# Performance work log

Measured on AMD Instinct MI355X. Metric: run time of the kernel, lower is better.

Reference implementation:

```python
import jax, jax.numpy as jnp
import numpy as np

B, T, D = 4, 2048, 1024
H = 16
HD = D // H

def setup_inputs() -> dict:
    key = jax.random.key(0)
    k1, k2, k3, k4, k5 = jax.random.split(key, 5)
    x = jax.random.normal(k1, (B, T, D), dtype=jnp.float32)
    scale = 1.0 / np.sqrt(D)
    W_qkv = jax.random.normal(k2, (D, 3 * D), dtype=jnp.float32) * scale
    b_qkv = jnp.zeros((3 * D,), dtype=jnp.float32)
    W_proj = jax.random.normal(k3, (D, D), dtype=jnp.float32) * scale
    b_proj = jnp.zeros((D,), dtype=jnp.float32)
    return {"x": x, "W_qkv": W_qkv, "b_qkv": b_qkv, "W_proj": W_proj, "b_proj": b_proj}

def reference(x, W_qkv, b_qkv, W_proj, b_proj):
    Bx, Tx, C = x.shape
    qkv = x @ W_qkv + b_qkv                      # [B,T,3C]
    q, k, v = jnp.split(qkv, 3, axis=-1)
    # [B,T,H,hd] -> [B,H,T,hd]
    q = q.reshape(Bx, Tx, H, HD).transpose(0, 2, 1, 3)
    k = k.reshape(Bx, Tx, H, HD).transpose(0, 2, 1, 3)
    v = v.reshape(Bx, Tx, H, HD).transpose(0, 2, 1, 3)
    att = jnp.einsum('bhqd,bhkd->bhqk', q, k) / jnp.sqrt(jnp.float32(HD))
    causal = jnp.tril(jnp.ones((Tx, Tx), dtype=bool))
    att = jnp.where(causal[None, None], att, -jnp.inf)
    att = jax.nn.softmax(att, axis=-1)
    y = jnp.einsum('bhqk,bhkd->bhqd', att, v)    # [B,H,T,hd]
    y = y.transpose(0, 2, 1, 3).reshape(Bx, Tx, C)
    return y @ W_proj + b_proj
```

## Files before the change

### kernel.cpp

```cpp
#include <hip/hip_runtime.h>
#include <hip/hip_bf16.h>

#define B_  4
#define T_  2048
#define D_  1024
#define H_  16
#define HD_ 64

typedef short s16x8 __attribute__((ext_vector_type(8)));
typedef short s16x4 __attribute__((ext_vector_type(4)));
typedef float f32x4 __attribute__((ext_vector_type(4)));
typedef unsigned int u32x2 __attribute__((ext_vector_type(2)));

#define MFMA32(a, b, c) __builtin_amdgcn_mfma_f32_16x16x32_bf16(a, b, c, 0, 0, 0)
#define MFMA16(a, b, c) __builtin_amdgcn_mfma_f32_16x16x16bf16_1k(a, b, c, 0, 0, 0)

__device__ __forceinline__ unsigned short f2bf(float f) {
  unsigned u = __builtin_bit_cast(unsigned, f);
  u += 0x7fffu + ((u >> 16) & 1u);
  return (unsigned short)(u >> 16);
}

__device__ __forceinline__ float bf2f(unsigned short h) {
  return __builtin_bit_cast(float, (unsigned)h << 16);
}

#define GLOAD_LDS16(src, dst)                                            \
  __builtin_amdgcn_global_load_lds(                                      \
      (__attribute__((address_space(1))) void*)(void*)(src),             \
      (__attribute__((address_space(3))) void*)(dst), 16, 0, 0)

__global__ __launch_bounds__(256) void convert_x_kernel(
    const float* __restrict__ in, unsigned short* __restrict__ out, int n8) {
  int i = blockIdx.x * 256 + threadIdx.x;
  if (i >= n8) return;
  const float4* p = ((const float4*)in) + (size_t)i * 2;
  float4 a = p[0], b = p[1];
  s16x8 o;
  o[0] = (short)f2bf(a.x); o[1] = (short)f2bf(a.y);
  o[2] = (short)f2bf(a.z); o[3] = (short)f2bf(a.w);
  o[4] = (short)f2bf(b.x); o[5] = (short)f2bf(b.y);
  o[6] = (short)f2bf(b.z); o[7] = (short)f2bf(b.w);
  *(((s16x8*)out) + i) = o;
}

__global__ __launch_bounds__(256) void transpose_w_kernel(
    const float* __restrict__ W, unsigned short* __restrict__ Wt, int K, int N) {
  __shared__ float tile[32][33];
  int n0 = blockIdx.x * 32, k0 = blockIdx.y * 32;
  int tx = threadIdx.x & 31, ty = threadIdx.x >> 5;
#pragma unroll
  for (int j = 0; j < 4; ++j) {
    int k = ty + j * 8;
    tile[k][tx] = W[(size_t)(k0 + k) * N + n0 + tx];
  }
  __syncthreads();
#pragma unroll
  for (int j = 0; j < 4; ++j) {
    int n = ty + j * 8;
    Wt[(size_t)(n0 + n) * K + k0 + tx] = f2bf(tile[tx][n]);
  }
}

template <int OUTF32>
__global__ __launch_bounds__(256) void gemm_kernel(
    const unsigned short* __restrict__ A, const unsigned short* __restrict__ Bt,
    const float* __restrict__ bias, void* __restrict__ Cout, int M, int N, int K) {
  __shared__ char lds[32768];
  char* Al = lds;
  char* Bl = lds + 16384;
  const int n0 = blockIdx.x * 128, m0 = blockIdx.y * 128;
  const int w = threadIdx.x >> 6, lane = threadIdx.x & 63;
  const int l15 = lane & 15, g = lane >> 4;
  const int wr = w >> 1, wc = w & 1;
  const int srow = (lane >> 3);
  const int u = lane & 7;
  f32x4 acc[4][4] = {};

  for (int kt = 0; kt < K; kt += 64) {
    __syncthreads();
#pragma unroll
    for (int i = 0; i < 4; ++i) {
      int c = w * 4 + i;
      int row = c * 8 + srow;
      const unsigned short* srcA = A + (size_t)(m0 + row) * K + kt + u * 8;
      GLOAD_LDS16(srcA, Al + c * 1024);
      const unsigned short* srcB = Bt + (size_t)(n0 + row) * K + kt + u * 8;
      GLOAD_LDS16(srcB, Bl + c * 1024);
    }
    __syncthreads();
#pragma unroll
    for (int kk = 0; kk < 2; ++kk) {
      s16x8 af[4], bfr[4];
#pragma unroll
      for (int mi = 0; mi < 4; ++mi) {
        int row = wr * 64 + mi * 16 + l15;
        af[mi] = *(const s16x8*)(Al + row * 128 + kk * 64 + g * 16);
      }
#pragma unroll
      for (int ni = 0; ni < 4; ++ni) {
        int row = wc * 64 + ni * 16 + l15;
        bfr[ni] = *(const s16x8*)(Bl + row * 128 + kk * 64 + g * 16);
      }
#pragma unroll
      for (int mi = 0; mi < 4; ++mi)
#pragma unroll
        for (int ni = 0; ni < 4; ++ni)
          acc[mi][ni] = MFMA32(af[mi], bfr[ni], acc[mi][ni]);
    }
  }
#pragma unroll
  for (int ni = 0; ni < 4; ++ni) {
    int col = n0 + wc * 64 + ni * 16 + l15;
    float bv = bias[col];
#pragma unroll
    for (int mi = 0; mi < 4; ++mi) {
      int row = m0 + wr * 64 + mi * 16 + g * 4;
#pragma unroll
      for (int r = 0; r < 4; ++r) {
        float v = acc[mi][ni][r] + bv;
        if (OUTF32)
          ((float*)Cout)[(size_t)(row + r) * N + col] = v;
        else
          ((unsigned short*)Cout)[(size_t)(row + r) * N + col] = f2bf(v);
      }
    }
  }
}

__global__ __launch_bounds__(256, 4) void attn_kernel(
    const unsigned short* __restrict__ qkv, unsigned short* __restrict__ yatt) {
  __shared__ char lds[8192 + 9344];
  const int bx = blockIdx.x;
  const int bh = blockIdx.y;
  const int b = bh >> 4, h = bh & 15;
  const int w = threadIdx.x >> 6;
  const int lane = threadIdx.x & 63;
  const int l15 = lane & 15, g = lane >> 4;

  const size_t rowstride = 3 * D_;
  const unsigned short* Qb = qkv + (size_t)b * T_ * rowstride + h * HD_;
  const unsigned short* Kb = Qb + D_;
  const unsigned short* Vb = Qb + 2 * D_;

  char* Klds = lds;
  unsigned short* Vt = (unsigned short*)(lds + 8192);

  const int krow0 = (w * 2 + 0) * 8 + (lane >> 3);
  const int krow1 = (w * 2 + 1) * 8 + (lane >> 3);
  const int u = lane & 7;
  const int vkey = w * 16 + (lane >> 2);
  const int vdb = lane & 3;
  const float SC = 0.18033688011112042f;

  s16x8 kreg0, kreg1, vreg0, vreg1;
  auto load_kv = [&](int kt) {
    const unsigned short* kb = Kb + (size_t)(kt * 64) * rowstride;
    kreg0 = *(const s16x8*)(kb + (size_t)krow0 * rowstride + u * 8);
    kreg1 = *(const s16x8*)(kb + (size_t)krow1 * rowstride + u * 8);
    const unsigned short* vs = Vb + (size_t)(kt * 64 + vkey) * rowstride + vdb * 16;
    vreg0 = *(const s16x8*)(vs);
    vreg1 = *(const s16x8*)(vs + 8);
  };

  load_kv(0);
#pragma unroll 1
  for (int ti = 0; ti < 2; ++ti) {
    const int qt = ti ? bx : 31 - bx;
    s16x8 qf0, qf1;
    {
      const unsigned short* qr = Qb + (size_t)(qt * 64 + w * 16 + l15) * rowstride;
      s16x8 a0 = *(const s16x8*)(qr + g * 8);
      s16x8 a1 = *(const s16x8*)(qr + 32 + g * 8);
#pragma unroll
      for (int j = 0; j < 8; ++j) {
        qf0[j] = (short)f2bf(bf2f((unsigned short)a0[j]) * SC);
        qf1[j] = (short)f2bf(bf2f((unsigned short)a1[j]) * SC);
      }
    }
    float m = -1e30f, rs = 0.f;
    f32x4 acc[4] = {};

#pragma unroll 1
    for (int kt = 0; kt <= qt; ++kt) {
      __syncthreads();
      *(s16x8*)(Klds + krow0 * 128 + ((u ^ (krow0 & 7)) << 4)) = kreg0;
      *(s16x8*)(Klds + krow1 * 128 + ((u ^ (krow1 & 7)) << 4)) = kreg1;
#pragma unroll
      for (int j = 0; j < 8; ++j) {
        Vt[vdb * 1168 + j * 72 + vkey] = (unsigned short)vreg0[j];
        Vt[vdb * 1168 + (8 + j) * 72 + vkey] = (unsigned short)vreg1[j];
      }
      __syncthreads();
      if (kt < qt) load_kv(kt + 1);
      else if (ti == 0) load_kv(0);

      float tv[16];
#pragma unroll
      for (int kk = 0; kk < 4; ++kk) {
        int key = kk * 16 + l15;
        const s16x8 kf0 = *(const s16x8*)(Klds + key * 128 + ((g ^ (key & 7)) << 4));
        const s16x8 kf1 = *(const s16x8*)(Klds + key * 128 + (((4 + g) ^ (key & 7)) << 4));
        f32x4 s = {};
        s = MFMA32(kf0, qf0, s);
        s = MFMA32(kf1, qf1, s);
#pragma unroll
        for (int r = 0; r < 4; ++r) tv[kk * 4 + r] = s[r];
      }
      if (kt == qt) {
        int q = qt * 64 + w * 16 + l15;
#pragma unroll
        for (int kk = 0; kk < 4; ++kk)
#pragma unroll
          for (int r = 0; r < 4; ++r)
            if (kt * 64 + kk * 16 + g * 4 + r > q) tv[kk * 4 + r] = -1e30f;
      }
      float tm = tv[0];
#pragma unroll
      for (int i = 1; i < 16; ++i) tm = fmaxf(tm, tv[i]);
      tm = fmaxf(tm, __shfl_xor(tm, 16));
      tm = fmaxf(tm, __shfl_xor(tm, 32));
      if (!__all(tm - m <= 8.0f)) {
        float mn = fmaxf(m, tm);
        float corr = exp2f(m - mn);
        m = mn;
        rs *= corr;
#pragma unroll
        for (int i = 0; i < 4; ++i) {
          acc[i][0] *= corr; acc[i][1] *= corr; acc[i][2] *= corr; acc[i][3] *= corr;
        }
      }
      s16x4 pb[4];
      float ps = 0.f;
#pragma unroll
      for (int kk = 0; kk < 4; ++kk) {
        float p0 = exp2f(tv[kk * 4 + 0] - m), p1 = exp2f(tv[kk * 4 + 1] - m);
        float p2 = exp2f(tv[kk * 4 + 2] - m), p3 = exp2f(tv[kk * 4 + 3] - m);
        ps += (p0 + p1) + (p2 + p3);
        u32x2 pk;
        pk[0] = __builtin_amdgcn_perm(__builtin_bit_cast(unsigned, p1),
                                      __builtin_bit_cast(unsigned, p0), 0x07060302u);
        pk[1] = __builtin_amdgcn_perm(__builtin_bit_cast(unsigned, p3),
                                      __builtin_bit_cast(unsigned, p2), 0x07060302u);
        pb[kk] = __builtin_bit_cast(s16x4, pk);
      }
      rs += ps;
#pragma unroll
      for (int kk = 0; kk < 4; ++kk) {
#pragma unroll
        for (int db = 0; db < 4; ++db) {
          s16x4 vf = *(const s16x4*)(Vt + db * 1168 + l15 * 72 + kk * 16 + g * 4);
          acc[db] = MFMA16(vf, pb[kk], acc[db]);
        }
      }
    }

    float rtot = rs + __shfl_xor(rs, 16);
    rtot += __shfl_xor(rtot, 32);
    float inv = 1.0f / rtot;
    __syncthreads();
    unsigned short* ylds = (unsigned short*)lds;
#pragma unroll
    for (int db = 0; db < 4; ++db)
#pragma unroll
      for (int r = 0; r < 4; ++r)
        ylds[(db * 16 + g * 4 + r) * 66 + w * 16 + l15] = f2bf(acc[db][r] * inv);
    __syncthreads();
    int qq = threadIdx.x >> 2;
    int dc = (threadIdx.x & 3) * 16;
    s16x8 o1, o2;
#pragma unroll
    for (int j = 0; j < 8; ++j) {
      o1[j] = (short)ylds[(dc + j) * 66 + qq];
      o2[j] = (short)ylds[(dc + 8 + j) * 66 + qq];
    }
    unsigned short* dst = yatt + (size_t)(b * T_ + qt * 64 + qq) * D_ + h * HD_ + dc;
    *(s16x8*)(dst) = o1;
    *(s16x8*)(dst + 8) = o2;
  }
}

extern "C" void kernel_launch(void* const* d_in, const int* in_sizes, int n_in,
                              void* d_out, int out_size, void* d_ws, size_t ws_size,
                              hipStream_t stream) {
  const float* x     = (const float*)d_in[0];
  const float* Wqkv  = (const float*)d_in[1];
  const float* bqkv  = (const float*)d_in[2];
  const float* Wproj = (const float*)d_in[3];
  const float* bproj = (const float*)d_in[4];
  float* out = (float*)d_out;

  unsigned short* xb   = (unsigned short*)d_ws;
  unsigned short* Wqb  = xb + (size_t)8192 * 1024;
  unsigned short* Wpb  = Wqb + (size_t)3072 * 1024;
  unsigned short* qkvb = Wpb + (size_t)1024 * 1024;
  unsigned short* yb   = xb;

  convert_x_kernel<<<dim3(4096), dim3(256), 0, stream>>>(x, xb, 8192 * 1024 / 8);
  transpose_w_kernel<<<dim3(96, 32), dim3(256), 0, stream>>>(Wqkv, Wqb, 1024, 3072);
  transpose_w_kernel<<<dim3(32, 32), dim3(256), 0, stream>>>(Wproj, Wpb, 1024, 1024);
  gemm_kernel<0><<<dim3(24, 64), dim3(256), 0, stream>>>(xb, Wqb, bqkv, qkvb, 8192, 3072, 1024);
  attn_kernel<<<dim3(16, 64), dim3(256), 0, stream>>>(qkvb, yb);
  gemm_kernel<1><<<dim3(8, 64), dim3(256), 0, stream>>>(yb, Wpb, bproj, out, 8192, 1024, 1024);
}
```

Baseline: 210.0 us.

## Widen attention query tile to 128 rows with 8 waves sharing each K/V tile

New measurement: 393.8 us. 87.5% more time.

```diff
diff --git a/kernel.cpp b/kernel.cpp
--- a/kernel.cpp
+++ b/kernel.cpp
@@ -128,14 +128,16 @@
   }
 }
 
-__global__ __launch_bounds__(256, 4) void attn_kernel(
+#define VT_STR 66
+__global__ __launch_bounds__(512, 4) void attn_kernel(
     const unsigned short* __restrict__ qkv, unsigned short* __restrict__ yatt) {
-  __shared__ char lds[8192 + 9344];
+  __shared__ char lds[16640];
   const int bx = blockIdx.x;
   const int bh = blockIdx.y;
   const int b = bh >> 4, h = bh & 15;
-  const int w = threadIdx.x >> 6;
-  const int lane = threadIdx.x & 63;
+  const int tid = threadIdx.x;
+  const int w = tid >> 6;
+  const int lane = tid & 63;
   const int l15 = lane & 15, g = lane >> 4;
 
   const size_t rowstride = 3 * D_;
@@ -146,30 +148,25 @@
   char* Klds = lds;
   unsigned short* Vt = (unsigned short*)(lds + 8192);
 
-  const int krow0 = (w * 2 + 0) * 8 + (lane >> 3);
-  const int krow1 = (w * 2 + 1) * 8 + (lane >> 3);
-  const int u = lane & 7;
-  const int vkey = w * 16 + (lane >> 2);
-  const int vdb = lane & 3;
+  const int srow = tid >> 3;
+  const int oct = tid & 7;
+  const int koff0 = (g ^ (l15 & 7)) << 4;
+  const int koff1 = ((4 + g) ^ (l15 & 7)) << 4;
   const float SC = 0.18033688011112042f;
 
-  s16x8 kreg0, kreg1, vreg0, vreg1;
+  s16x8 kreg, vreg;
   auto load_kv = [&](int kt) {
-    const unsigned short* kb = Kb + (size_t)(kt * 64) * rowstride;
-    kreg0 = *(const s16x8*)(kb + (size_t)krow0 * rowstride + u * 8);
-    kreg1 = *(const s16x8*)(kb + (size_t)krow1 * rowstride + u * 8);
-    const unsigned short* vs = Vb + (size_t)(kt * 64 + vkey) * rowstride + vdb * 16;
-    vreg0 = *(const s16x8*)(vs);
-    vreg1 = *(const s16x8*)(vs + 8);
+    kreg = *(const s16x8*)(Kb + (size_t)(kt * 64 + srow) * rowstride + oct * 8);
+    vreg = *(const s16x8*)(Vb + (size_t)(kt * 64 + srow) * rowstride + oct * 8);
   };
 
   load_kv(0);
 #pragma unroll 1
   for (int ti = 0; ti < 2; ++ti) {
-    const int qt = ti ? bx : 31 - bx;
+    const int qt = ti ? bx : 15 - bx;
     s16x8 qf0, qf1;
     {
-      const unsigned short* qr = Qb + (size_t)(qt * 64 + w * 16 + l15) * rowstride;
+      const unsigned short* qr = Qb + (size_t)(qt * 128 + w * 16 + l15) * rowstride;
       s16x8 a0 = *(const s16x8*)(qr + g * 8);
       s16x8 a1 = *(const s16x8*)(qr + 32 + g * 8);
 #pragma unroll
@@ -180,77 +177,84 @@
     }
     float m = -1e30f, rs = 0.f;
     f32x4 acc[4] = {};
+    const int ktmax = 2 * qt + 1;
 
 #pragma unroll 1
-    for (int kt = 0; kt <= qt; ++kt) {
+    for (int kt = 0; kt <= ktmax; ++kt) {
       __syncthreads();
-      *(s16x8*)(Klds + krow0 * 128 + ((u ^ (krow0 & 7)) << 4)) = kreg0;
-      *(s16x8*)(Klds + krow1 * 128 + ((u ^ (krow1 & 7)) << 4)) = kreg1;
-#pragma unroll
-      for (int j = 0; j < 8; ++j) {
-        Vt[vdb * 1168 + j * 72 + vkey] = (unsigned short)vreg0[j];
-        Vt[vdb * 1168 + (8 + j) * 72 + vkey] = (unsigned short)vreg1[j];
-      }
+      *(s16x8*)(Klds + srow * 128 + ((oct ^ (srow & 7)) << 4)) = kreg;
+#pragma unroll
+      for (int j = 0; j < 8; ++j)
+        Vt[(oct * 8 + j) * VT_STR + srow] = (unsigned short)vreg[j];
       __syncthreads();
-      if (kt < qt) load_kv(kt + 1);
+      if (kt < ktmax) load_kv(kt + 1);
       else if (ti == 0) load_kv(0);
 
-      float tv[16];
-#pragma unroll
-      for (int kk = 0; kk < 4; ++kk) {
-        int key = kk * 16 + l15;
-        const s16x8 kf0 = *(const s16x8*)(Klds + key * 128 + ((g ^ (key & 7)) << 4));
-        const s16x8 kf1 = *(const s16x8*)(Klds + key * 128 + (((4 + g) ^ (key & 7)) << 4));
-        f32x4 s = {};
-        s = MFMA32(kf0, qf0, s);
-        s = MFMA32(kf1, qf1, s);
-#pragma unroll
-        for (int r = 0; r < 4; ++r) tv[kk * 4 + r] = s[r];
-      }
-      if (kt == qt) {
-        int q = qt * 64 + w * 16 + l15;
-#pragma unroll
-        for (int kk = 0; kk < 4; ++kk)
-#pragma unroll
-          for (int r = 0; r < 4; ++r)
-            if (kt * 64 + kk * 16 + g * 4 + r > q) tv[kk * 4 + r] = -1e30f;
-      }
-      float tm = tv[0];
-#pragma unroll
-      for (int i = 1; i < 16; ++i) tm = fmaxf(tm, tv[i]);
-      tm = fmaxf(tm, __shfl_xor(tm, 16));
-      tm = fmaxf(tm, __shfl_xor(tm, 32));
-      if (!__all(tm - m <= 8.0f)) {
-        float mn = fmaxf(m, tm);
-        float corr = exp2f(m - mn);
-        m = mn;
-        rs *= corr;
-#pragma unroll
-        for (int i = 0; i < 4; ++i) {
-          acc[i][0] *= corr; acc[i][1] *= corr; acc[i][2] *= corr; acc[i][3] *= corr;
-        }
-      }
-      s16x4 pb[4];
-      float ps = 0.f;
-#pragma unroll
-      for (int kk = 0; kk < 4; ++kk) {
-        float p0 = exp2f(tv[kk * 4 + 0] - m), p1 = exp2f(tv[kk * 4 + 1] - m);
-        float p2 = exp2f(tv[kk * 4 + 2] - m), p3 = exp2f(tv[kk * 4 + 3] - m);
-        ps += (p0 + p1) + (p2 + p3);
-        u32x2 pk;
-        pk[0] = __builtin_amdgcn_perm(__builtin_bit_cast(unsigned, p1),
-                                      __builtin_bit_cast(unsigned, p0), 0x07060302u);
-        pk[1] = __builtin_amdgcn_perm(__builtin_bit_cast(unsigned, p3),
-                                      __builtin_bit_cast(unsigned, p2), 0x07060302u);
-        pb[kk] = __builtin_bit_cast(s16x4, pk);
-      }
-      rs += ps;
-#pragma unroll
-      for (int kk = 0; kk < 4; ++kk) {
-#pragma unroll
-        for (int db = 0; db < 4; ++db) {
-          s16x4 vf = *(const s16x4*)(Vt + db * 1168 + l15 * 72 + kk * 16 + g * 4);
-          acc[db] = MFMA16(vf, pb[kk], acc[db]);
+      const bool skip = (kt * 64 > qt * 128 + w * 16 + 15);
+      if (!skip) {
+        float tv[16];
+        const char* kbase = Klds + l15 * 128;
+#pragma unroll
+        for (int kk = 0; kk < 4; ++kk) {
+          const s16x8 kf0 = *(const s16x8*)(kbase + kk * 2048 + koff0);
+          const s16x8 kf1 = *(const s16x8*)(kbase + kk * 2048 + koff1);
+          f32x4 s = {};
+          s = MFMA32(kf0, qf0, s);
+          s = MFMA32(kf1, qf1, s);
+#pragma unroll
+          for (int r = 0; r < 4; ++r) tv[kk * 4 + r] = s[r];
+        }
+        if (kt * 64 + 63 > qt * 128 + w * 16) {
+          int q = qt * 128 + w * 16 + l15;
+#pragma unroll
+          for (int kk = 0; kk < 4; ++kk)
+#pragma unroll
+            for (int r = 0; r < 4; ++r)
+              if (kt * 64 + kk * 16 + g * 4 + r > q) tv[kk * 4 + r] = -1e30f;
+        }
+        float x0 = fmaxf(tv[0], tv[1]), x1 = fmaxf(tv[2], tv[3]);
+        float x2 = fmaxf(tv[4], tv[5]), x3 = fmaxf(tv[6], tv[7]);
+        float x4 = fmaxf(tv[8], tv[9]), x5 = fmaxf(tv[10], tv[11]);
+        float x6 = fmaxf(tv[12], tv[13]), x7 = fmaxf(tv[14], tv[15]);
+        float y0 = fmaxf(fmaxf(x0, x1), fmaxf(x2, x3));
+        float y1 = fmaxf(fmaxf(x4, x5), fmaxf(x6, x7));
+        float tm = fmaxf(y0, y1);
+        tm = fmaxf(tm, __shfl_xor(tm, 16));
+        tm = fmaxf(tm, __shfl_xor(tm, 32));
+        if (!__all(tm - m <= 8.0f)) {
+          float mn = fmaxf(m, tm);
+          float corr = exp2f(m - mn);
+          m = mn;
+          rs *= corr;
+#pragma unroll
+          for (int i = 0; i < 4; ++i) {
+            acc[i][0] *= corr; acc[i][1] *= corr;
+            acc[i][2] *= corr; acc[i][3] *= corr;
+          }
+        }
+        s16x4 pb[4];
+        float ps = 0.f;
+#pragma unroll
+        for (int kk = 0; kk < 4; ++kk) {
+          float p0 = exp2f(tv[kk * 4 + 0] - m), p1 = exp2f(tv[kk * 4 + 1] - m);
+          float p2 = exp2f(tv[kk * 4 + 2] - m), p3 = exp2f(tv[kk * 4 + 3] - m);
+          ps += (p0 + p1) + (p2 + p3);
+          u32x2 pk;
+          pk[0] = __builtin_amdgcn_perm(__builtin_bit_cast(unsigned, p1),
+                                        __builtin_bit_cast(unsigned, p0), 0x07060302u);
+          pk[1] = __builtin_amdgcn_perm(__builtin_bit_cast(unsigned, p3),
+                                        __builtin_bit_cast(unsigned, p2), 0x07060302u);
+          pb[kk] = __builtin_bit_cast(s16x4, pk);
+        }
+        rs += ps;
+#pragma unroll
+        for (int kk = 0; kk < 4; ++kk) {
+#pragma unroll
+          for (int db = 0; db < 4; ++db) {
+            s16x4 vf =
+                *(const s16x4*)(Vt + (db * 16 + l15) * VT_STR + kk * 16 + g * 4);
+            acc[db] = MFMA16(vf, pb[kk], acc[db]);
+          }
         }
       }
     }
@@ -264,19 +268,22 @@
     for (int db = 0; db < 4; ++db)
 #pragma unroll
       for (int r = 0; r < 4; ++r)
-        ylds[(db * 16 + g * 4 + r) * 66 + w * 16 + l15] = f2bf(acc[db][r] * inv);
+        ylds[(db * 16 + g * 4 + r) * 130 + w * 16 + l15] = f2bf(acc[db][r] * inv);
     __syncthreads();
-    int qq = threadIdx.x >> 2;
-    int dc = (threadIdx.x & 3) * 16;
-    s16x8 o1, o2;
-#pragma unroll
-    for (int j = 0; j < 8; ++j) {
-      o1[j] = (short)ylds[(dc + j) * 66 + qq];
-      o2[j] = (short)ylds[(dc + 8 + j) * 66 + qq];
-    }
-    unsigned short* dst = yatt + (size_t)(b * T_ + qt * 64 + qq) * D_ + h * HD_ + dc;
-    *(s16x8*)(dst) = o1;
-    *(s16x8*)(dst + 8) = o2;
+    {
+      int qq = tid >> 2;
+      int dc = (tid & 3) * 16;
+      s16x8 o1, o2;
+#pragma unroll
+      for (int j = 0; j < 8; ++j) {
+        o1[j] = (short)ylds[(dc + j) * 130 + qq];
+        o2[j] = (short)ylds[(dc + 8 + j) * 130 + qq];
+      }
+      unsigned short* dst =
+          yatt + (size_t)(b * T_ + qt * 128 + qq) * D_ + h * HD_ + dc;
+      *(s16x8*)(dst) = o1;
+      *(s16x8*)(dst + 8) = o2;
+    }
   }
 }
 
@@ -300,6 +307,6 @@
   transpose_w_kernel<<<dim3(96, 32), dim3(256), 0, stream>>>(Wqkv, Wqb, 1024, 3072);
   transpose_w_kernel<<<dim3(32, 32), dim3(256), 0, stream>>>(Wproj, Wpb, 1024, 1024);
   gemm_kernel<0><<<dim3(24, 64), dim3(256), 0, stream>>>(xb, Wqb, bqkv, qkvb, 8192, 3072, 1024);
-  attn_kernel<<<dim3(16, 64), dim3(256), 0, stream>>>(qkvb, yb);
+  attn_kernel<<<dim3(8, 64), dim3(512), 0, stream>>>(qkvb, yb);
   gemm_kernel<1><<<dim3(8, 64), dim3(256), 0, stream>>>(yb, Wpb, bproj, out, 8192, 1024, 1024);
 }
```
